# Performance work log

Hardware: AMD Instinct MI355X
Metric: run time of the kernel (lower is better)

## Reference

```python
import jax, jax.numpy as jnp
import numpy as np

B, C, T_TEXT, T_FEAT = 32, 256, 512, 2048
DELTA = 0.1  # self.temperature


def setup_inputs() -> dict:
    key = jax.random.key(0)
    k1, k2 = jax.random.split(key)
    x = jax.random.normal(k1, (B, C, T_TEXT), dtype=jnp.float32)
    # token durations in frames, ~U[0, 8): avg ~4 frames/token -> T_FEAT ~ 2048
    w = jax.random.uniform(k2, (B, T_TEXT), dtype=jnp.float32) * 8.0
    x_mask = jnp.ones((B, T_TEXT), dtype=bool)
    y_mask = jnp.ones((B, T_FEAT), dtype=bool)
    return {"x": x, "w": w, "x_mask": x_mask, "y_mask": y_mask}


def reference(x, w, x_mask, y_mask):
    # Gaussian upsampling (arXiv 2010.04301) with fixed temperature DELTA.
    # x: (B, C, T_text), w: (B, T_text), x_mask: (B, T_text), y_mask: (B, T_feat)
    T_feats = y_mask.shape[-1]
    # frame time indices, zeroed where y_mask is False
    t = jnp.arange(T_feats, dtype=jnp.float32)[None, :] * y_mask.astype(jnp.float32)  # (B, T_feat)
    # Gaussian centers: cumulative duration minus half of own duration
    c = jnp.cumsum(w, axis=-1) - 0.5 * w  # (B, T_text)
    # energy: -delta * (t - c)^2  -> (B, T_feat, T_text)
    energy = -DELTA * (t[:, :, None] - c[:, None, :]) ** 2
    # mask out padded text tokens
    energy = jnp.where(x_mask[:, None, :], energy, -jnp.inf)
    p_attn = jax.nn.softmax(energy, axis=-1)  # (B, T_feat, T_text)
    # weighted sum over text tokens: (B, C, T_feat)
    out = jnp.einsum("btn,bcn->bct", p_attn, x)
    return out
```

## Files before the change

kernel.cpp:

```cpp
#include <hip/hip_runtime.h>
#include <hip/hip_bf16.h>

#define B_    32
#define C_    256
#define NT    512
#define TFEAT 2048
#define TT    32
#define UW    96
#define PRE   32
#define DELTA 0.1f

typedef __attribute__((ext_vector_type(4))) float f32x4;
typedef __attribute__((ext_vector_type(8))) unsigned short u16x8;
typedef __attribute__((ext_vector_type(8))) __bf16 bf16x8;

static __device__ inline unsigned short f2bfbits(float f) {
    __bf16 h = (__bf16)f;
    return __builtin_bit_cast(unsigned short, h);
}
static __device__ inline float bf2f(unsigned short h) {
    return __uint_as_float(((unsigned)h) << 16);
}

__global__ __launch_bounds__(256) void prep_kernel(const float* __restrict__ w,
                                                   float* __restrict__ cout,
                                                   int* __restrict__ lotab) {
    __shared__ float cs[NT];
    __shared__ float wsum[8];
    int tid  = threadIdx.x;
    int b    = blockIdx.x;
    int lane = tid & 63;
    int wv   = tid >> 6;

    float v0 = w[b * NT + tid];
    float v1 = w[b * NT + 256 + tid];
    float s0 = v0, s1 = v1;
#pragma unroll
    for (int off = 1; off < 64; off <<= 1) {
        float t0 = __shfl_up(s0, off);
        float t1 = __shfl_up(s1, off);
        if (lane >= off) { s0 += t0; s1 += t1; }
    }
    if (lane == 63) { wsum[wv] = s0; wsum[4 + wv] = s1; }
    __syncthreads();
    float pre0 = 0.f;
    float pre1 = wsum[0] + wsum[1] + wsum[2] + wsum[3];
#pragma unroll
    for (int i = 0; i < 4; ++i) if (i < wv) pre0 += wsum[i];
#pragma unroll
    for (int i = 0; i < 4; ++i) if (i < wv) pre1 += wsum[4 + i];
    float c0 = pre0 + s0 - 0.5f * v0;
    float c1 = pre1 + s1 - 0.5f * v1;
    cs[tid]       = c0;
    cs[256 + tid] = c1;
    cout[b * NT + tid]       = c0;
    cout[b * NT + 256 + tid] = c1;
    __syncthreads();

    if (tid < TFEAT / TT) {
        float ft = (float)(tid * TT);
        int lo = 0, hi = NT;
        while (hi > lo) {
            int mid = (lo + hi) >> 1;
            if (cs[mid] < ft) lo = mid + 1; else hi = mid;
        }
        int n1 = lo < NT - 1 ? lo : NT - 1;
        int n0 = lo - 1 > 0 ? lo - 1 : 0;
        int nstar = (fabsf(ft - cs[n0]) <= fabsf(ft - cs[n1])) ? n0 : n1;
        int L = (nstar - PRE) & ~3;
        if (L < 0) L = 0;
        if (L > NT - UW) L = NT - UW;
        lotab[b * (TFEAT / TT) + tid] = L;
    }
}

__global__ __launch_bounds__(64) void g_kernel(const float* __restrict__ x,
                                               const float* __restrict__ cw,
                                               const int* __restrict__ lotab,
                                               float* __restrict__ out) {
    int bx   = blockIdx.x;
    int b    = bx & 31;
    int tile = bx >> 5;
    int l    = threadIdx.x;
    int fr   = l & 15;
    int kg   = l >> 4;
    int LO   = lotab[b * (TFEAT / TT) + tile];
    int t0   = tile * TT;

    const float* cp = cw + b * NT + LO + kg * 8;
    f32x4 cv[6];
#pragma unroll
    for (int ks = 0; ks < 3; ++ks) {
        cv[2 * ks]     = *reinterpret_cast<const f32x4*>(cp + ks * 32);
        cv[2 * ks + 1] = *reinterpret_cast<const f32x4*>(cp + ks * 32 + 4);
    }

    float ft0 = (float)(t0 + fr);
    float ft1 = (float)(t0 + 16 + fr);
    float e0[24], e1[24];
    float mx0 = -1e30f, mx1 = -1e30f;
#pragma unroll
    for (int ks = 0; ks < 3; ++ks)
#pragma unroll
        for (int q = 0; q < 8; ++q) {
            float c = cv[2 * ks + (q >> 2)][q & 3];
            float d0 = ft0 - c, d1 = ft1 - c;
            float a0 = -DELTA * d0 * d0;
            float a1 = -DELTA * d1 * d1;
            e0[ks * 8 + q] = a0; mx0 = fmaxf(mx0, a0);
            e1[ks * 8 + q] = a1; mx1 = fmaxf(mx1, a1);
        }
    mx0 = fmaxf(mx0, __shfl_xor(mx0, 16)); mx0 = fmaxf(mx0, __shfl_xor(mx0, 32));
    mx1 = fmaxf(mx1, __shfl_xor(mx1, 16)); mx1 = fmaxf(mx1, __shfl_xor(mx1, 32));

    bf16x8 af0[3], af1[3];
    float sum0 = 0.f, sum1 = 0.f;
#pragma unroll
    for (int ks = 0; ks < 3; ++ks)
#pragma unroll
        for (int q = 0; q < 8; ++q) {
            unsigned short p0 = f2bfbits(__expf(e0[ks * 8 + q] - mx0));
            unsigned short p1 = f2bfbits(__expf(e1[ks * 8 + q] - mx1));
            sum0 += bf2f(p0);
            sum1 += bf2f(p1);
            af0[ks][q] = __builtin_bit_cast(__bf16, p0);
            af1[ks][q] = __builtin_bit_cast(__bf16, p1);
        }
    sum0 += __shfl_xor(sum0, 16); sum0 += __shfl_xor(sum0, 32);
    sum1 += __shfl_xor(sum1, 16); sum1 += __shfl_xor(sum1, 32);
    float inv0 = 1.f / fmaxf(sum0, 1e-30f);
    float inv1 = 1.f / fmaxf(sum1, 1e-30f);

    f32x4 sv0, sv1;
#pragma unroll
    for (int r = 0; r < 4; ++r) {
        sv0[r] = __shfl(inv0, kg * 4 + r);
        sv1[r] = __shfl(inv1, kg * 4 + r);
    }

    const float* xbase = x + ((size_t)b * C_) * NT + LO + kg * 8;
    float* ob = out + ((size_t)b * C_) * TFEAT + t0 + kg * 4;

#pragma unroll 2
    for (int ct = 0; ct < 16; ++ct) {
        const float* xr = xbase + (size_t)(ct * 16 + fr) * NT;
        bf16x8 bfr[3];
#pragma unroll
        for (int ks = 0; ks < 3; ++ks) {
            f32x4 a0 = *reinterpret_cast<const f32x4*>(xr + ks * 32);
            f32x4 a1 = *reinterpret_cast<const f32x4*>(xr + ks * 32 + 4);
            bf16x8 vv;
#pragma unroll
            for (int q = 0; q < 4; ++q) {
                vv[q]     = (__bf16)a0[q];
                vv[q + 4] = (__bf16)a1[q];
            }
            bfr[ks] = vv;
        }
        f32x4 acc0 = (f32x4){0.f, 0.f, 0.f, 0.f};
        f32x4 acc1 = (f32x4){0.f, 0.f, 0.f, 0.f};
#pragma unroll
        for (int ks = 0; ks < 3; ++ks) {
            acc0 = __builtin_amdgcn_mfma_f32_16x16x32_bf16(af0[ks], bfr[ks], acc0, 0, 0, 0);
            acc1 = __builtin_amdgcn_mfma_f32_16x16x32_bf16(af1[ks], bfr[ks], acc1, 0, 0, 0);
        }
        float* op = ob + (size_t)(ct * 16 + fr) * TFEAT;
        __builtin_nontemporal_store(acc0 * sv0, reinterpret_cast<f32x4*>(op));
        __builtin_nontemporal_store(acc1 * sv1, reinterpret_cast<f32x4*>(op + 16));
    }
}

extern "C" void kernel_launch(void* const* d_in, const int* in_sizes, int n_in,
                              void* d_out, int out_size, void* d_ws, size_t ws_size,
                              hipStream_t stream) {
    const float* x = (const float*)d_in[0];
    const float* w = (const float*)d_in[1];
    float* out  = (float*)d_out;
    float* cbuf = (float*)d_ws;
    int*   lotab = (int*)((char*)d_ws + 65536);

    hipLaunchKernelGGL(prep_kernel, dim3(B_), dim3(256), 0, stream, w, cbuf, lotab);
    hipLaunchKernelGGL(g_kernel, dim3(B_ * (TFEAT / TT)), dim3(64), 0, stream,
                       x, cbuf, lotab, out);
}
```

Measured before the change: 36.38 us.

## Fuse prefix-sum prep into main kernel and prefetch x rows in registers

```diff
diff --git a/kernel.cpp b/kernel.cpp
--- a/kernel.cpp
+++ b/kernel.cpp
@@ -22,77 +22,62 @@
     return __uint_as_float(((unsigned)h) << 16);
 }
 
-__global__ __launch_bounds__(256) void prep_kernel(const float* __restrict__ w,
-                                                   float* __restrict__ cout,
-                                                   int* __restrict__ lotab) {
+__global__ __launch_bounds__(64, 2) void fused_kernel(const float* __restrict__ x,
+                                                      const float* __restrict__ w,
+                                                      float* __restrict__ out) {
     __shared__ float cs[NT];
-    __shared__ float wsum[8];
-    int tid  = threadIdx.x;
-    int b    = blockIdx.x;
-    int lane = tid & 63;
-    int wv   = tid >> 6;
 
-    float v0 = w[b * NT + tid];
-    float v1 = w[b * NT + 256 + tid];
-    float s0 = v0, s1 = v1;
-#pragma unroll
-    for (int off = 1; off < 64; off <<= 1) {
-        float t0 = __shfl_up(s0, off);
-        float t1 = __shfl_up(s1, off);
-        if (lane >= off) { s0 += t0; s1 += t1; }
-    }
-    if (lane == 63) { wsum[wv] = s0; wsum[4 + wv] = s1; }
-    __syncthreads();
-    float pre0 = 0.f;
-    float pre1 = wsum[0] + wsum[1] + wsum[2] + wsum[3];
-#pragma unroll
-    for (int i = 0; i < 4; ++i) if (i < wv) pre0 += wsum[i];
-#pragma unroll
-    for (int i = 0; i < 4; ++i) if (i < wv) pre1 += wsum[4 + i];
-    float c0 = pre0 + s0 - 0.5f * v0;
-    float c1 = pre1 + s1 - 0.5f * v1;
-    cs[tid]       = c0;
-    cs[256 + tid] = c1;
-    cout[b * NT + tid]       = c0;
-    cout[b * NT + 256 + tid] = c1;
-    __syncthreads();
-
-    if (tid < TFEAT / TT) {
-        float ft = (float)(tid * TT);
-        int lo = 0, hi = NT;
-        while (hi > lo) {
-            int mid = (lo + hi) >> 1;
-            if (cs[mid] < ft) lo = mid + 1; else hi = mid;
-        }
-        int n1 = lo < NT - 1 ? lo : NT - 1;
-        int n0 = lo - 1 > 0 ? lo - 1 : 0;
-        int nstar = (fabsf(ft - cs[n0]) <= fabsf(ft - cs[n1])) ? n0 : n1;
-        int L = (nstar - PRE) & ~3;
-        if (L < 0) L = 0;
-        if (L > NT - UW) L = NT - UW;
-        lotab[b * (TFEAT / TT) + tid] = L;
-    }
-}
-
-__global__ __launch_bounds__(64) void g_kernel(const float* __restrict__ x,
-                                               const float* __restrict__ cw,
-                                               const int* __restrict__ lotab,
-                                               float* __restrict__ out) {
     int bx   = blockIdx.x;
     int b    = bx & 31;
     int tile = bx >> 5;
     int l    = threadIdx.x;
     int fr   = l & 15;
     int kg   = l >> 4;
-    int LO   = lotab[b * (TFEAT / TT) + tile];
     int t0   = tile * TT;
 
-    const float* cp = cw + b * NT + LO + kg * 8;
+    float v[8], sc[8];
+    const float* wp = w + b * NT + l;
+#pragma unroll
+    for (int k = 0; k < 8; ++k) v[k] = wp[64 * k];
+    float carry = 0.f;
+#pragma unroll
+    for (int k = 0; k < 8; ++k) {
+        float s = v[k];
+#pragma unroll
+        for (int off = 1; off < 64; off <<= 1) {
+            float t = __shfl_up(s, off);
+            if (l >= off) s += t;
+        }
+        sc[k] = carry + s - 0.5f * v[k];
+        carry += __shfl(s, 63);
+    }
+#pragma unroll
+    for (int k = 0; k < 8; ++k) cs[64 * k + l] = sc[k];
+    __syncthreads();
+
+    float ft = (float)t0;
+    float dmin = 1e30f; int nmin = 0;
+#pragma unroll
+    for (int k = 0; k < 8; ++k) {
+        float d = fabsf(ft - sc[k]);
+        if (d < dmin) { dmin = d; nmin = 64 * k + l; }
+    }
+#pragma unroll
+    for (int off = 32; off >= 1; off >>= 1) {
+        float od = __shfl_xor(dmin, off);
+        int   on = __shfl_xor(nmin, off);
+        if (od < dmin || (od == dmin && on < nmin)) { dmin = od; nmin = on; }
+    }
+    int LO = (nmin - PRE) & ~3;
+    LO = LO < 0 ? 0 : LO;
+    LO = LO > NT - UW ? NT - UW : LO;
+    LO = __builtin_amdgcn_readfirstlane(LO);
+
     f32x4 cv[6];
 #pragma unroll
     for (int ks = 0; ks < 3; ++ks) {
-        cv[2 * ks]     = *reinterpret_cast<const f32x4*>(cp + ks * 32);
-        cv[2 * ks + 1] = *reinterpret_cast<const f32x4*>(cp + ks * 32 + 4);
+        cv[2 * ks]     = *reinterpret_cast<const f32x4*>(&cs[LO + kg * 8 + ks * 32]);
+        cv[2 * ks + 1] = *reinterpret_cast<const f32x4*>(&cs[LO + kg * 8 + ks * 32 + 4]);
     }
 
     float ft0 = (float)(t0 + fr);
@@ -141,22 +126,35 @@
     const float* xbase = x + ((size_t)b * C_) * NT + LO + kg * 8;
     float* ob = out + ((size_t)b * C_) * TFEAT + t0 + kg * 4;
 
-#pragma unroll 2
+    f32x4 st[4][6];
+    auto issue = [&](int ct, int buf) {
+        const float* xr = xbase + (size_t)(ct * 16 + fr) * NT;
+#pragma unroll
+        for (int ks = 0; ks < 3; ++ks) {
+            st[buf][2 * ks]     = *reinterpret_cast<const f32x4*>(xr + ks * 32);
+            st[buf][2 * ks + 1] = *reinterpret_cast<const f32x4*>(xr + ks * 32 + 4);
+        }
+    };
+
+    issue(0, 0); issue(1, 1); issue(2, 2);
+
+#pragma unroll
     for (int ct = 0; ct < 16; ++ct) {
-        const float* xr = xbase + (size_t)(ct * 16 + fr) * NT;
+        int cb = ct & 3;
+        if (ct + 3 < 16) issue(ct + 3, (ct + 3) & 3);
+
         bf16x8 bfr[3];
 #pragma unroll
         for (int ks = 0; ks < 3; ++ks) {
-            f32x4 a0 = *reinterpret_cast<const f32x4*>(xr + ks * 32);
-            f32x4 a1 = *reinterpret_cast<const f32x4*>(xr + ks * 32 + 4);
             bf16x8 vv;
 #pragma unroll
             for (int q = 0; q < 4; ++q) {
-                vv[q]     = (__bf16)a0[q];
-                vv[q + 4] = (__bf16)a1[q];
+                vv[q]     = (__bf16)st[cb][2 * ks][q];
+                vv[q + 4] = (__bf16)st[cb][2 * ks + 1][q];
             }
             bfr[ks] = vv;
         }
+
         f32x4 acc0 = (f32x4){0.f, 0.f, 0.f, 0.f};
         f32x4 acc1 = (f32x4){0.f, 0.f, 0.f, 0.f};
 #pragma unroll
@@ -164,6 +162,7 @@
             acc0 = __builtin_amdgcn_mfma_f32_16x16x32_bf16(af0[ks], bfr[ks], acc0, 0, 0, 0);
             acc1 = __builtin_amdgcn_mfma_f32_16x16x32_bf16(af1[ks], bfr[ks], acc1, 0, 0, 0);
         }
+
         float* op = ob + (size_t)(ct * 16 + fr) * TFEAT;
         __builtin_nontemporal_store(acc0 * sv0, reinterpret_cast<f32x4*>(op));
         __builtin_nontemporal_store(acc1 * sv1, reinterpret_cast<f32x4*>(op + 16));
@@ -175,11 +174,8 @@
                               hipStream_t stream) {
     const float* x = (const float*)d_in[0];
     const float* w = (const float*)d_in[1];
-    float* out  = (float*)d_out;
-    float* cbuf = (float*)d_ws;
-    int*   lotab = (int*)((char*)d_ws + 65536);
+    float* out = (float*)d_out;
 
-    hipLaunchKernelGGL(prep_kernel, dim3(B_), dim3(256), 0, stream, w, cbuf, lotab);
-    hipLaunchKernelGGL(g_kernel, dim3(B_ * (TFEAT / TT)), dim3(64), 0, stream,
-                       x, cbuf, lotab, out);
+    hipLaunchKernelGGL(fused_kernel, dim3(B_ * (TFEAT / TT)), dim3(64), 0, stream,
+                       x, w, out);
 }
```

After: 36.82 us. Within noise of the previous version (+1.2%).

## Fuse prefix-sum prep into main kernel and stage x as bf16 in LDS

Applied to the files above, without the earlier changes.

```diff
diff --git a/kernel.cpp b/kernel.cpp
--- a/kernel.cpp
+++ b/kernel.cpp
@@ -9,9 +9,11 @@
 #define UW    96
 #define PRE   32
 #define DELTA 0.1f
+#define CG    16
+#define XSTR  520
 
 typedef __attribute__((ext_vector_type(4))) float f32x4;
-typedef __attribute__((ext_vector_type(8))) unsigned short u16x8;
+typedef __attribute__((ext_vector_type(4))) __bf16 bf16x4;
 typedef __attribute__((ext_vector_type(8))) __bf16 bf16x8;
 
 static __device__ inline unsigned short f2bfbits(float f) {
@@ -22,24 +24,35 @@
     return __uint_as_float(((unsigned)h) << 16);
 }
 
-__global__ __launch_bounds__(256) void prep_kernel(const float* __restrict__ w,
-                                                   float* __restrict__ cout,
-                                                   int* __restrict__ lotab) {
+__global__ __launch_bounds__(256, 2) void fused_kernel(const float* __restrict__ x,
+                                                       const float* __restrict__ w,
+                                                       float* __restrict__ out) {
     __shared__ float cs[NT];
     __shared__ float wsum[8];
+    __shared__ int sLO[TFEAT / TT];
+    __shared__ __bf16 xsbf[CG][XSTR];
+
     int tid  = threadIdx.x;
-    int b    = blockIdx.x;
+    int bx   = blockIdx.x;
+    int b    = bx & 31;
+    int cg   = bx >> 5;
     int lane = tid & 63;
     int wv   = tid >> 6;
+
+    const float* xg = x + ((size_t)(b * C_ + cg * CG)) * NT;
+    f32x4 xr[8];
+#pragma unroll
+    for (int q = 0; q < 8; ++q)
+        xr[q] = *reinterpret_cast<const f32x4*>(xg + wv * 2048 + q * 256 + lane * 4);
 
     float v0 = w[b * NT + tid];
     float v1 = w[b * NT + 256 + tid];
     float s0 = v0, s1 = v1;
 #pragma unroll
     for (int off = 1; off < 64; off <<= 1) {
-        float t0 = __shfl_up(s0, off);
-        float t1 = __shfl_up(s1, off);
-        if (lane >= off) { s0 += t0; s1 += t1; }
+        float u0 = __shfl_up(s0, off);
+        float u1 = __shfl_up(s1, off);
+        if (lane >= off) { s0 += u0; s1 += u1; }
     }
     if (lane == 63) { wsum[wv] = s0; wsum[4 + wv] = s1; }
     __syncthreads();
@@ -49,12 +62,8 @@
     for (int i = 0; i < 4; ++i) if (i < wv) pre0 += wsum[i];
 #pragma unroll
     for (int i = 0; i < 4; ++i) if (i < wv) pre1 += wsum[4 + i];
-    float c0 = pre0 + s0 - 0.5f * v0;
-    float c1 = pre1 + s1 - 0.5f * v1;
-    cs[tid]       = c0;
-    cs[256 + tid] = c1;
-    cout[b * NT + tid]       = c0;
-    cout[b * NT + 256 + tid] = c1;
+    cs[tid]       = pre0 + s0 - 0.5f * v0;
+    cs[256 + tid] = pre1 + s1 - 0.5f * v1;
     __syncthreads();
 
     if (tid < TFEAT / TT) {
@@ -67,96 +76,88 @@
         int n1 = lo < NT - 1 ? lo : NT - 1;
         int n0 = lo - 1 > 0 ? lo - 1 : 0;
         int nstar = (fabsf(ft - cs[n0]) <= fabsf(ft - cs[n1])) ? n0 : n1;
-        int L = (nstar - PRE) & ~3;
+        int L = (nstar - PRE) & ~7;
         if (L < 0) L = 0;
         if (L > NT - UW) L = NT - UW;
-        lotab[b * (TFEAT / TT) + tid] = L;
-    }
-}
-
-__global__ __launch_bounds__(64) void g_kernel(const float* __restrict__ x,
-                                               const float* __restrict__ cw,
-                                               const int* __restrict__ lotab,
-                                               float* __restrict__ out) {
-    int bx   = blockIdx.x;
-    int b    = bx & 31;
-    int tile = bx >> 5;
-    int l    = threadIdx.x;
-    int fr   = l & 15;
-    int kg   = l >> 4;
-    int LO   = lotab[b * (TFEAT / TT) + tile];
-    int t0   = tile * TT;
-
-    const float* cp = cw + b * NT + LO + kg * 8;
-    f32x4 cv[6];
-#pragma unroll
-    for (int ks = 0; ks < 3; ++ks) {
-        cv[2 * ks]     = *reinterpret_cast<const f32x4*>(cp + ks * 32);
-        cv[2 * ks + 1] = *reinterpret_cast<const f32x4*>(cp + ks * 32 + 4);
+        sLO[tid] = L;
     }
 
-    float ft0 = (float)(t0 + fr);
-    float ft1 = (float)(t0 + 16 + fr);
-    float e0[24], e1[24];
-    float mx0 = -1e30f, mx1 = -1e30f;
 #pragma unroll
-    for (int ks = 0; ks < 3; ++ks)
+    for (int q = 0; q < 8; ++q) {
+        int f   = wv * 2048 + q * 256 + lane * 4;
+        int row = f >> 9;
+        int col = f & 511;
+        bf16x4 hv;
 #pragma unroll
-        for (int q = 0; q < 8; ++q) {
-            float c = cv[2 * ks + (q >> 2)][q & 3];
-            float d0 = ft0 - c, d1 = ft1 - c;
-            float a0 = -DELTA * d0 * d0;
-            float a1 = -DELTA * d1 * d1;
-            e0[ks * 8 + q] = a0; mx0 = fmaxf(mx0, a0);
-            e1[ks * 8 + q] = a1; mx1 = fmaxf(mx1, a1);
-        }
-    mx0 = fmaxf(mx0, __shfl_xor(mx0, 16)); mx0 = fmaxf(mx0, __shfl_xor(mx0, 32));
-    mx1 = fmaxf(mx1, __shfl_xor(mx1, 16)); mx1 = fmaxf(mx1, __shfl_xor(mx1, 32));
+        for (int e = 0; e < 4; ++e) hv[e] = (__bf16)xr[q][e];
+        *reinterpret_cast<bf16x4*>(&xsbf[row][col]) = hv;
+    }
+    __syncthreads();
 
-    bf16x8 af0[3], af1[3];
-    float sum0 = 0.f, sum1 = 0.f;
-#pragma unroll
-    for (int ks = 0; ks < 3; ++ks)
-#pragma unroll
-        for (int q = 0; q < 8; ++q) {
-            unsigned short p0 = f2bfbits(__expf(e0[ks * 8 + q] - mx0));
-            unsigned short p1 = f2bfbits(__expf(e1[ks * 8 + q] - mx1));
-            sum0 += bf2f(p0);
-            sum1 += bf2f(p1);
-            af0[ks][q] = __builtin_bit_cast(__bf16, p0);
-            af1[ks][q] = __builtin_bit_cast(__bf16, p1);
-        }
-    sum0 += __shfl_xor(sum0, 16); sum0 += __shfl_xor(sum0, 32);
-    sum1 += __shfl_xor(sum1, 16); sum1 += __shfl_xor(sum1, 32);
-    float inv0 = 1.f / fmaxf(sum0, 1e-30f);
-    float inv1 = 1.f / fmaxf(sum1, 1e-30f);
-
-    f32x4 sv0, sv1;
-#pragma unroll
-    for (int r = 0; r < 4; ++r) {
-        sv0[r] = __shfl(inv0, kg * 4 + r);
-        sv1[r] = __shfl(inv1, kg * 4 + r);
-    }
-
-    const float* xbase = x + ((size_t)b * C_) * NT + LO + kg * 8;
-    float* ob = out + ((size_t)b * C_) * TFEAT + t0 + kg * 4;
+    int fr = lane & 15;
+    int kg = lane >> 4;
 
 #pragma unroll 2
-    for (int ct = 0; ct < 16; ++ct) {
-        const float* xr = xbase + (size_t)(ct * 16 + fr) * NT;
+    for (int i = 0; i < 16; ++i) {
+        int tile = wv * 16 + i;
+        int t0   = tile * TT;
+        int LO   = sLO[tile];
+
+        f32x4 cv[6];
+#pragma unroll
+        for (int ks = 0; ks < 3; ++ks) {
+            cv[2 * ks]     = *reinterpret_cast<const f32x4*>(&cs[LO + kg * 8 + ks * 32]);
+            cv[2 * ks + 1] = *reinterpret_cast<const f32x4*>(&cs[LO + kg * 8 + ks * 32 + 4]);
+        }
+
         bf16x8 bfr[3];
 #pragma unroll
-        for (int ks = 0; ks < 3; ++ks) {
-            f32x4 a0 = *reinterpret_cast<const f32x4*>(xr + ks * 32);
-            f32x4 a1 = *reinterpret_cast<const f32x4*>(xr + ks * 32 + 4);
-            bf16x8 vv;
+        for (int ks = 0; ks < 3; ++ks)
+            bfr[ks] = *reinterpret_cast<const bf16x8*>(&xsbf[fr][LO + ks * 32 + kg * 8]);
+
+        float ft0 = (float)(t0 + fr);
+        float ft1 = (float)(t0 + 16 + fr);
+        float e0[24], e1[24];
+        float mx0 = -1e30f, mx1 = -1e30f;
 #pragma unroll
-            for (int q = 0; q < 4; ++q) {
-                vv[q]     = (__bf16)a0[q];
-                vv[q + 4] = (__bf16)a1[q];
+        for (int ks = 0; ks < 3; ++ks)
+#pragma unroll
+            for (int q = 0; q < 8; ++q) {
+                float c = cv[2 * ks + (q >> 2)][q & 3];
+                float d0 = ft0 - c, d1 = ft1 - c;
+                float a0 = -DELTA * d0 * d0;
+                float a1 = -DELTA * d1 * d1;
+                e0[ks * 8 + q] = a0; mx0 = fmaxf(mx0, a0);
+                e1[ks * 8 + q] = a1; mx1 = fmaxf(mx1, a1);
             }
-            bfr[ks] = vv;
+        mx0 = fmaxf(mx0, __shfl_xor(mx0, 16)); mx0 = fmaxf(mx0, __shfl_xor(mx0, 32));
+        mx1 = fmaxf(mx1, __shfl_xor(mx1, 16)); mx1 = fmaxf(mx1, __shfl_xor(mx1, 32));
+
+        bf16x8 af0[3], af1[3];
+        float sum0 = 0.f, sum1 = 0.f;
+#pragma unroll
+        for (int ks = 0; ks < 3; ++ks)
+#pragma unroll
+            for (int q = 0; q < 8; ++q) {
+                unsigned short p0 = f2bfbits(__expf(e0[ks * 8 + q] - mx0));
+                unsigned short p1 = f2bfbits(__expf(e1[ks * 8 + q] - mx1));
+                sum0 += bf2f(p0);
+                sum1 += bf2f(p1);
+                af0[ks][q] = __builtin_bit_cast(__bf16, p0);
+                af1[ks][q] = __builtin_bit_cast(__bf16, p1);
+            }
+        sum0 += __shfl_xor(sum0, 16); sum0 += __shfl_xor(sum0, 32);
+        sum1 += __shfl_xor(sum1, 16); sum1 += __shfl_xor(sum1, 32);
+        float inv0 = 1.f / fmaxf(sum0, 1e-30f);
+        float inv1 = 1.f / fmaxf(sum1, 1e-30f);
+
+        f32x4 sv0, sv1;
+#pragma unroll
+        for (int r = 0; r < 4; ++r) {
+            sv0[r] = __shfl(inv0, kg * 4 + r);
+            sv1[r] = __shfl(inv1, kg * 4 + r);
         }
+
         f32x4 acc0 = (f32x4){0.f, 0.f, 0.f, 0.f};
         f32x4 acc1 = (f32x4){0.f, 0.f, 0.f, 0.f};
 #pragma unroll
@@ -164,7 +165,8 @@
             acc0 = __builtin_amdgcn_mfma_f32_16x16x32_bf16(af0[ks], bfr[ks], acc0, 0, 0, 0);
             acc1 = __builtin_amdgcn_mfma_f32_16x16x32_bf16(af1[ks], bfr[ks], acc1, 0, 0, 0);
         }
-        float* op = ob + (size_t)(ct * 16 + fr) * TFEAT;
+
+        float* op = out + ((size_t)(b * C_ + cg * CG + fr)) * TFEAT + t0 + kg * 4;
         __builtin_nontemporal_store(acc0 * sv0, reinterpret_cast<f32x4*>(op));
         __builtin_nontemporal_store(acc1 * sv1, reinterpret_cast<f32x4*>(op + 16));
     }
@@ -175,11 +177,8 @@
                               hipStream_t stream) {
     const float* x = (const float*)d_in[0];
     const float* w = (const float*)d_in[1];
-    float* out  = (float*)d_out;
-    float* cbuf = (float*)d_ws;
-    int*   lotab = (int*)((char*)d_ws + 65536);
+    float* out = (float*)d_out;
 
-    hipLaunchKernelGGL(prep_kernel, dim3(B_), dim3(256), 0, stream, w, cbuf, lotab);
-    hipLaunchKernelGGL(g_kernel, dim3(B_ * (TFEAT / TT)), dim3(64), 0, stream,
-                       x, cbuf, lotab, out);
+    hipLaunchKernelGGL(fused_kernel, dim3(B_ * CG), dim3(256), 0, stream,
+                       x, w, out);
 }
```

Measured after the change: 43.37 us. 1.19x slower.
